# Kernel tuning notes

Measured on AMD Instinct MI355X. Metric: run time of the kernel, lower is better.

## Reference

```python
import jax, jax.numpy as jnp
import numpy as np

SEQ_LEN = 2_000_000
NUM_TAGS = 50


def setup_inputs() -> dict:
    key = jax.random.key(0)
    k1, k2, k3 = jax.random.split(key, 3)
    logits = jax.random.normal(k1, (SEQ_LEN, NUM_TAGS), dtype=jnp.float32)
    tags = jax.random.randint(k2, (SEQ_LEN,), 0, NUM_TAGS, dtype=jnp.int64)
    # learned parameter from __init__: transitions ~ randn(num_tags, num_tags)
    transitions = jax.random.normal(k3, (NUM_TAGS, NUM_TAGS), dtype=jnp.float32)
    return {"logits": logits, "tags": tags, "transitions": transitions}


def reference(logits, tags, transitions):
    # score = sum_i logits[i, tags[i]] + sum_{i>0} transitions[tags[i-1], tags[i]]
    # forward returns -score (negative path score, used as the loss)
    emit = jnp.take_along_axis(logits, tags[:, None], axis=1).sum()  # [S] gather -> scalar
    trans = transitions[tags[:-1], tags[1:]].sum()                   # [S-1] gather -> scalar
    return -(emit + trans)
```

## Files before the change

### kernel.cpp

```cpp
#include <hip/hip_runtime.h>


#define NUM_TAGS 50

__global__ __launch_bounds__(256) void crf_score_kernel(
    const float* __restrict__ logits,
    const int*   __restrict__ tags,
    const float* __restrict__ trans,
    float* __restrict__ out,
    int n)
{
    __shared__ float s_trans[NUM_TAGS * NUM_TAGS];
    for (int i = threadIdx.x; i < NUM_TAGS * NUM_TAGS; i += blockDim.x)
        s_trans[i] = trans[i];
    __syncthreads();

    const int tid = blockIdx.x * blockDim.x + threadIdx.x;
    const long long i0 = (long long)tid * 4;

    float acc = 0.0f;
    if (i0 < n) {
        int t0, t1, t2, t3;
        if (i0 + 3 < n) {
            int4 tv = *(const int4*)(tags + i0);
            t0 = tv.x; t1 = tv.y; t2 = tv.z; t3 = tv.w;
        } else {
            t0 = tags[i0];
            t1 = (i0 + 1 < n) ? tags[i0 + 1] : 0;
            t2 = (i0 + 2 < n) ? tags[i0 + 2] : 0;
            t3 = (i0 + 3 < n) ? tags[i0 + 3] : 0;
        }

        const float* row = logits + i0 * NUM_TAGS;
        float e0 = row[t0];
        float e1 = (i0 + 1 < n) ? row[NUM_TAGS + t1]     : 0.0f;
        float e2 = (i0 + 2 < n) ? row[2 * NUM_TAGS + t2] : 0.0f;
        float e3 = (i0 + 3 < n) ? row[3 * NUM_TAGS + t3] : 0.0f;
        acc = e0 + e1 + e2 + e3;

        if (i0 + 1 < n) acc += s_trans[t0 * NUM_TAGS + t1];
        if (i0 + 2 < n) acc += s_trans[t1 * NUM_TAGS + t2];
        if (i0 + 3 < n) acc += s_trans[t2 * NUM_TAGS + t3];
        if (i0 + 4 < n) {
            int t4 = tags[i0 + 4];
            acc += s_trans[t3 * NUM_TAGS + t4];
        }
    }

    #pragma unroll
    for (int off = 32; off > 0; off >>= 1)
        acc += __shfl_down(acc, off, 64);

    __shared__ float s_part[4];
    int lane = threadIdx.x & 63;
    int wid  = threadIdx.x >> 6;
    if (lane == 0) s_part[wid] = acc;
    __syncthreads();

    if (wid == 0) {
        float v = (lane < 4) ? s_part[lane] : 0.0f;
        #pragma unroll
        for (int off = 2; off > 0; off >>= 1)
            v += __shfl_down(v, off, 64);
        if (lane == 0)
            atomicAdd(out, -v);
    }
}

extern "C" void kernel_launch(void* const* d_in, const int* in_sizes, int n_in,
                              void* d_out, int out_size, void* d_ws, size_t ws_size,
                              hipStream_t stream) {
    const float* logits = (const float*)d_in[0];
    const int*   tags   = (const int*)d_in[1];
    const float* trans  = (const float*)d_in[2];
    float* out = (float*)d_out;
    int n = in_sizes[1];

    hipMemsetAsync(out, 0, sizeof(float), stream);

    const int block = 256;
    const int threads_needed = (n + 3) / 4;
    const int grid = (threads_needed + block - 1) / block;
    crf_score_kernel<<<grid, block, 0, stream>>>(logits, tags, trans, out, n);
}
```

Baseline: 492.8 us.

## Stream logits tiles through LDS with coalesced vector loads in persistent blocks

Replaces the scattered per-row gather of logits with fully coalesced 16-byte loads of whole 256-row tiles into shared memory, followed by gathers from LDS. The grid becomes persistent, capped at 512 blocks that loop over tiles, so the transition table is loaded and the atomic issued only once per block. This reads every logits element, the whole 400MB array, rather than only the cache lines that hold gathered entries. Since rows are 200 bytes, the gather already touches most lines, so total traffic may not drop while the 51KB LDS footprint limits occupancy.

```diff
diff --git a/kernel.cpp b/kernel.cpp
--- a/kernel.cpp
+++ b/kernel.cpp
@@ -2,48 +2,70 @@
 
 
 #define NUM_TAGS 50
+#define TILE 256
+#define THREADS 256
+#define VEC_PER_TILE ((TILE * NUM_TAGS) / 4)
+#define LOADS_PER_THREAD ((VEC_PER_TILE + THREADS - 1) / THREADS)
 
-__global__ __launch_bounds__(256) void crf_score_kernel(
+__global__ __launch_bounds__(THREADS) void crf_score_kernel(
     const float* __restrict__ logits,
     const int*   __restrict__ tags,
     const float* __restrict__ trans,
     float* __restrict__ out,
     int n)
 {
+    __shared__ __align__(16) float s_log[TILE * NUM_TAGS];
     __shared__ float s_trans[NUM_TAGS * NUM_TAGS];
-    for (int i = threadIdx.x; i < NUM_TAGS * NUM_TAGS; i += blockDim.x)
+    __shared__ int   s_tags[TILE + 1];
+    __shared__ float s_part[THREADS / 64];
+
+    const int tid = threadIdx.x;
+
+    for (int i = tid; i < NUM_TAGS * NUM_TAGS; i += THREADS)
         s_trans[i] = trans[i];
-    __syncthreads();
 
-    const int tid = blockIdx.x * blockDim.x + threadIdx.x;
-    const long long i0 = (long long)tid * 4;
+    const int ntiles = (n + TILE - 1) / TILE;
+    float acc = 0.0f;
 
-    float acc = 0.0f;
-    if (i0 < n) {
-        int t0, t1, t2, t3;
-        if (i0 + 3 < n) {
-            int4 tv = *(const int4*)(tags + i0);
-            t0 = tv.x; t1 = tv.y; t2 = tv.z; t3 = tv.w;
-        } else {
-            t0 = tags[i0];
-            t1 = (i0 + 1 < n) ? tags[i0 + 1] : 0;
-            t2 = (i0 + 2 < n) ? tags[i0 + 2] : 0;
-            t3 = (i0 + 3 < n) ? tags[i0 + 3] : 0;
+    for (int tile = blockIdx.x; tile < ntiles; tile += gridDim.x) {
+        const long long base = (long long)tile * TILE;
+        const long long rem  = (long long)n - base;
+        const int rows = (rem < TILE) ? (int)rem : TILE;
+        const int nflt = rows * NUM_TAGS;
+        const int nvec = nflt >> 2;
+
+        const uint4* g = (const uint4*)(logits + base * NUM_TAGS);
+        uint4 r[LOADS_PER_THREAD];
+        #pragma unroll
+        for (int k = 0; k < LOADS_PER_THREAD; ++k) {
+            const int idx = tid + k * THREADS;
+            if (idx < nvec) r[k] = g[idx];
         }
+        int tg = 0;
+        if (tid < rows) tg = tags[base + tid];
+        int tgN = 0;
+        if (tid == 0 && base + rows < n) tgN = tags[base + rows];
 
-        const float* row = logits + i0 * NUM_TAGS;
-        float e0 = row[t0];
-        float e1 = (i0 + 1 < n) ? row[NUM_TAGS + t1]     : 0.0f;
-        float e2 = (i0 + 2 < n) ? row[2 * NUM_TAGS + t2] : 0.0f;
-        float e3 = (i0 + 3 < n) ? row[3 * NUM_TAGS + t3] : 0.0f;
-        acc = e0 + e1 + e2 + e3;
+        __syncthreads();
+        #pragma unroll
+        for (int k = 0; k < LOADS_PER_THREAD; ++k) {
+            const int idx = tid + k * THREADS;
+            if (idx < nvec) ((uint4*)s_log)[idx] = r[k];
+        }
+        for (int idx = (nvec << 2) + tid; idx < nflt; idx += THREADS)
+            s_log[idx] = logits[base * NUM_TAGS + idx];
+        if (tid < rows) s_tags[tid] = tg;
+        if (tid == 0)   s_tags[rows] = tgN;
+        __syncthreads();
 
-        if (i0 + 1 < n) acc += s_trans[t0 * NUM_TAGS + t1];
-        if (i0 + 2 < n) acc += s_trans[t1 * NUM_TAGS + t2];
-        if (i0 + 3 < n) acc += s_trans[t2 * NUM_TAGS + t3];
-        if (i0 + 4 < n) {
-            int t4 = tags[i0 + 4];
-            acc += s_trans[t3 * NUM_TAGS + t4];
+        if (tid < rows) {
+            const int t = s_tags[tid];
+            float v = s_log[tid * NUM_TAGS + t];
+            if (base + tid + 1 < n) {
+                const int t2 = s_tags[tid + 1];
+                v += s_trans[t * NUM_TAGS + t2];
+            }
+            acc += v;
         }
     }
 
@@ -51,14 +73,13 @@
     for (int off = 32; off > 0; off >>= 1)
         acc += __shfl_down(acc, off, 64);
 
-    __shared__ float s_part[4];
-    int lane = threadIdx.x & 63;
-    int wid  = threadIdx.x >> 6;
+    const int lane = tid & 63;
+    const int wid  = tid >> 6;
     if (lane == 0) s_part[wid] = acc;
     __syncthreads();
 
     if (wid == 0) {
-        float v = (lane < 4) ? s_part[lane] : 0.0f;
+        float v = (lane < THREADS / 64) ? s_part[lane] : 0.0f;
         #pragma unroll
         for (int off = 2; off > 0; off >>= 1)
             v += __shfl_down(v, off, 64);
@@ -74,12 +95,11 @@
     const int*   tags   = (const int*)d_in[1];
     const float* trans  = (const float*)d_in[2];
     float* out = (float*)d_out;
-    int n = in_sizes[1];
+    const int n = in_sizes[1];
 
     hipMemsetAsync(out, 0, sizeof(float), stream);
 
-    const int block = 256;
-    const int threads_needed = (n + 3) / 4;
-    const int grid = (threads_needed + block - 1) / block;
-    crf_score_kernel<<<grid, block, 0, stream>>>(logits, tags, trans, out, n);
+    const int ntiles = (n + TILE - 1) / TILE;
+    const int grid = (ntiles < 512) ? ntiles : 512;
+    crf_score_kernel<<<grid, THREADS, 0, stream>>>(logits, tags, trans, out, n);
 }
```

After: 689.9 us. +40.0%, slower.
